# Kernel optimization log

Measured on AMD Instinct MI355X. Metric: run time of the kernel, lower is better.

Reference implementation:

```python
import jax, jax.numpy as jnp
import numpy as np


def setup_inputs() -> dict:
    key = jax.random.key(0)
    k1, k2 = jax.random.split(key)
    B, C, H, W, D = 2, 1, 128, 128, 128
    image = jax.random.normal(k1, (B, C, H, W, D), dtype=jnp.float32)
    # dense displacement field in voxel units (typical registration magnitudes)
    ddf = jax.random.normal(k2, (B, 3, H, W, D), dtype=jnp.float32) * 3.0
    return {"image": image, "ddf": ddf}


def _warp(image, ddf):
    """Trilinear grid_sample warp, padding_mode='zeros', align_corners=True.

    Equivalent to MONAI Warp(mode=1, padding_mode='zeros'): the reference grid
    plus DDF gives absolute voxel coordinates; torch's normalization to [-1,1]
    with align_corners=True followed by grid_sample maps exactly back to these
    voxel coordinates, so we sample directly in voxel space.
    """
    B, C, H, W, D = image.shape
    dt = image.dtype
    mesh = jnp.stack(
        jnp.meshgrid(
            jnp.arange(H, dtype=dt),
            jnp.arange(W, dtype=dt),
            jnp.arange(D, dtype=dt),
            indexing="ij",
        ),
        axis=-1,
    )  # (H, W, D, 3)
    coords = mesh[None] + jnp.moveaxis(ddf, 1, -1)  # (B, H, W, D, 3) voxel coords

    c0f = jnp.floor(coords)
    frac = coords - c0f                      # (B, H, W, D, 3)
    c0 = c0f.astype(jnp.int32)
    sizes = jnp.array([H, W, D], dtype=jnp.int32)
    strides = jnp.array([W * D, D, 1], dtype=jnp.int32)

    N = H * W * D
    img_flat = image.reshape(B, C, N)
    out = jnp.zeros((B, C, N), dtype=dt)
    # 8 trilinear taps; zeros padding => out-of-range taps contribute 0
    for dx in (0, 1):
        for dy in (0, 1):
            for dz in (0, 1):
                off = jnp.array([dx, dy, dz], dtype=jnp.int32)
                idx = c0 + off                                   # (B,H,W,D,3)
                wsel = jnp.where(off == 1, frac, 1.0 - frac)
                w = wsel[..., 0] * wsel[..., 1] * wsel[..., 2]   # (B,H,W,D)
                valid = jnp.all((idx >= 0) & (idx < sizes), axis=-1)
                idxc = jnp.clip(idx, 0, sizes - 1)
                lin = jnp.sum(idxc * strides, axis=-1).reshape(B, N)
                vals = jax.vmap(lambda im, li: im[:, li])(img_flat, lin)  # (B,C,N)
                out = out + vals * (w * valid.astype(dt)).reshape(B, 1, N)
    return out.reshape(B, C, H, W, D)


def reference(image, ddf):
    return _warp(image, ddf)
```

## Files before the change

kernel.cpp:

```cpp
#include <hip/hip_runtime.h>
#include <hip/hip_fp16.h>


constexpr int H = 128, W = 128, D = 128;
constexpr int N = H * W * D;
constexpr int B = 2;
constexpr int HA = 8;
constexpr int RS = 32;
constexpr int RCELL = 18;
constexpr int RHALF = RCELL * 2;
constexpr int RN = RS * RS * RHALF;

typedef float fvec4 __attribute__((ext_vector_type(4)));
typedef unsigned u2v __attribute__((ext_vector_type(2), aligned(4)));
typedef unsigned u2v8 __attribute__((ext_vector_type(2), aligned(8)));

__global__ __launch_bounds__(1024, 8) void warp_tile_kernel(
    const float* __restrict__ image,
    const float* __restrict__ ddf,
    float* __restrict__ out)
{
    __shared__ __half tile[RN];

    int bid = blockIdx.x;
    int T   = (bid & 7) * 128 + (bid >> 3);
    int b  = T >> 9;
    int t3 = T & 511;
    int tx0 = ((t3 >> 6) & 7) << 4;
    int ty0 = ((t3 >> 3) & 7) << 4;
    int tz0 = (t3 & 7) << 4;
    int ox = tx0 - HA, oy = ty0 - HA, oz = tz0 - HA;

    const float* img = image + ((size_t)b << 21);
    int t = threadIdx.x;

    int zq = (t & 3) << 2;
    int ly = (t >> 2) & 15;
    int lx = t >> 6;
    int vx = tx0 + lx, vy = ty0 + ly, vz = tz0 + zq;
    int lin0 = (vx << 14) + (vy << 7) + vz;

    fvec4 sa[4], sb[4];
    int rows[4], zos[4];
#pragma unroll
    for (int c = 0; c < 4; ++c) {
        int s   = c * 1024 + t;
        int row = s >> 2;
        int zo  = (s & 3) << 3;
        rows[c] = row; zos[c] = zo;
        int gx = ox + (row >> 5);
        int gy = oy + (row & 31);
        int gz = oz + zo;
        bool ok = ((unsigned)gx < 128u) & ((unsigned)gy < 128u) & ((unsigned)gz < 121u);
        const float* p = img + (gx << 14) + (gy << 7) + gz;
        fvec4 z4 = {0.f, 0.f, 0.f, 0.f};
        sa[c] = ok ? *(const fvec4*)p       : z4;
        sb[c] = ok ? *(const fvec4*)(p + 4) : z4;
    }

    const float* ddfb = ddf + (size_t)b * 3 * N;
    fvec4 dx4 = *(const fvec4*)(ddfb + lin0);
    fvec4 dy4 = *(const fvec4*)(ddfb + lin0 + N);
    fvec4 dz4 = *(const fvec4*)(ddfb + lin0 + 2 * N);

    unsigned short* tp = (unsigned short*)tile;
#pragma unroll
    for (int c = 0; c < 4; ++c) {
        __half2 h0 = __floats2half2_rn(sa[c].x, sa[c].y);
        __half2 h1 = __floats2half2_rn(sa[c].z, sa[c].w);
        __half2 h2 = __floats2half2_rn(sb[c].x, sb[c].y);
        __half2 h3 = __floats2half2_rn(sb[c].z, sb[c].w);
        u2v8 w0, w1;
        w0.x = *(unsigned int*)&h0;
        w0.y = *(unsigned int*)&h1;
        w1.x = *(unsigned int*)&h2;
        w1.y = *(unsigned int*)&h3;
        unsigned short* dst = tp + rows[c] * RHALF + zos[c];
        *(u2v8*)dst       = w0;
        *(u2v8*)(dst + 4) = w1;
    }
    __syncthreads();

    __builtin_amdgcn_s_setprio(1);

    float* outb = out + ((size_t)b << 21);
    const unsigned int* cells = (const unsigned int*)tile;
    float dxp[4] = {dx4.x, dx4.y, dx4.z, dx4.w};
    float dyp[4] = {dy4.x, dy4.y, dy4.z, dy4.w};
    float dzp[4] = {dz4.x, dz4.y, dz4.z, dz4.w};
    float res[4];

#pragma unroll
    for (int i = 0; i < 4; ++i) {
        float x = (float)vx + dxp[i];
        float y = (float)vy + dyp[i];
        float z = (float)(vz + i) + dzp[i];

        float xf = floorf(x), yf = floorf(y), zf = floorf(z);
        float fx = x - xf, fy = y - yf, fz = z - zf;
        int x0 = (int)xf, y0 = (int)yf, z0 = (int)zf;
        int rx = x0 - ox, ry = y0 - oy, rz = z0 - oz;

        float acc;
        if ((unsigned)rx <= 30u && (unsigned)ry <= 30u && (unsigned)rz <= 30u) {
            int row = (rx << 5) + ry;
            int c   = row * RCELL + (rz >> 1);
            int sh  = (rz & 1) << 4;
            u2v q00 = *(const u2v*)(cells + c);
            u2v q01 = *(const u2v*)(cells + c + RCELL);
            u2v q10 = *(const u2v*)(cells + c + 32 * RCELL);
            u2v q11 = *(const u2v*)(cells + c + 33 * RCELL);

            float az0 = 1.f - fz;
            float zz[4];
            unsigned los[4] = {q00.x, q01.x, q10.x, q11.x};
            unsigned his[4] = {q00.y, q01.y, q10.y, q11.y};
#pragma unroll
            for (int p2 = 0; p2 < 4; ++p2) {
                unsigned pr = __builtin_amdgcn_alignbit(his[p2], los[p2],
                                                        (unsigned)sh);
                __half2 hp = *(__half2*)&pr;
                float2 f2 = __half22float2(hp);
                zz[p2] = az0 * f2.x + fz * f2.y;
            }
            float ay0 = 1.f - fy;
            acc = (1.f - fx) * (ay0 * zz[0] + fy * zz[1]) +
                  fx         * (ay0 * zz[2] + fy * zz[3]);
        } else {
            int x1 = x0 + 1, y1 = y0 + 1, z1 = z0 + 1;
            bool vx0 = (unsigned)x0 < (unsigned)H;
            bool vx1 = (unsigned)x1 < (unsigned)H;
            bool vy0 = (unsigned)y0 < (unsigned)W;
            bool vy1 = (unsigned)y1 < (unsigned)W;
            bool vz0 = (unsigned)z0 < (unsigned)D;
            bool vz1 = (unsigned)z1 < (unsigned)D;
            float ax0 = vx0 ? (1.0f - fx) : 0.0f;
            float ax1 = vx1 ? fx          : 0.0f;
            float ay0 = vy0 ? (1.0f - fy) : 0.0f;
            float ay1 = vy1 ? fy          : 0.0f;
            float az0 = vz0 ? (1.0f - fz) : 0.0f;
            float az1 = vz1 ? fz          : 0.0f;
            int cx0 = vx0 ? x0 : 0;
            int cx1 = vx1 ? x1 : 0;
            int cy0 = vy0 ? y0 : 0;
            int cy1 = vy1 ? y1 : 0;
            int cz0 = vz0 ? z0 : 0;
            int cz1 = vz1 ? z1 : 0;
            int rx0 = cx0 << 14, rx1 = cx1 << 14;
            int ry0 = cy0 << 7,  ry1 = cy1 << 7;
            float v000 = img[rx0 + ry0 + cz0];
            float v001 = img[rx0 + ry0 + cz1];
            float v010 = img[rx0 + ry1 + cz0];
            float v011 = img[rx0 + ry1 + cz1];
            float v100 = img[rx1 + ry0 + cz0];
            float v101 = img[rx1 + ry0 + cz1];
            float v110 = img[rx1 + ry1 + cz0];
            float v111 = img[rx1 + ry1 + cz1];
            acc = ax0 * (ay0 * (az0 * v000 + az1 * v001) +
                         ay1 * (az0 * v010 + az1 * v011)) +
                  ax1 * (ay0 * (az0 * v100 + az1 * v101) +
                         ay1 * (az0 * v110 + az1 * v111));
        }
        res[i] = acc;
    }
    __builtin_amdgcn_s_setprio(0);
    fvec4 r4 = {res[0], res[1], res[2], res[3]};
    __builtin_nontemporal_store(r4, (fvec4*)(outb + lin0));
}

extern "C" void kernel_launch(void* const* d_in, const int* in_sizes, int n_in,
                              void* d_out, int out_size, void* d_ws, size_t ws_size,
                              hipStream_t stream) {
    const float* image = (const float*)d_in[0];
    const float* ddf   = (const float*)d_in[1];
    float* out = (float*)d_out;

    warp_tile_kernel<<<B * 512, 1024, 0, stream>>>(image, ddf, out);
}
```

Measured before the change: 102.5 us.

## Process two x-adjacent tiles per block with ring-buffered halo reuse

Each block now handles two consecutive 16-wide x tiles, with half the grid size. The shared-memory halo is indexed modulo 32 in x, so the second tile reuses 16 of the 32 loaded x-planes and loads only 16 new ones. The loads for the second tile's new planes are issued before the first tile's compute so their latency overlaps it. This cuts redundant halo loads from global memory and overlaps loading with compute, but it halves the number of blocks and adds extra barriers and register pressure.

```diff
diff --git a/kernel.cpp b/kernel.cpp
--- a/kernel.cpp
+++ b/kernel.cpp
@@ -5,11 +5,9 @@
 constexpr int H = 128, W = 128, D = 128;
 constexpr int N = H * W * D;
 constexpr int B = 2;
-constexpr int HA = 8;
-constexpr int RS = 32;
 constexpr int RCELL = 18;
 constexpr int RHALF = RCELL * 2;
-constexpr int RN = RS * RS * RHALF;
+constexpr int RN = 1024 * RHALF;
 
 typedef float fvec4 __attribute__((ext_vector_type(4)));
 typedef unsigned u2v __attribute__((ext_vector_type(2), aligned(4)));
@@ -23,149 +21,210 @@
     __shared__ __half tile[RN];
 
     int bid = blockIdx.x;
-    int T   = (bid & 7) * 128 + (bid >> 3);
-    int b  = T >> 9;
-    int t3 = T & 511;
-    int tx0 = ((t3 >> 6) & 7) << 4;
+    int T   = (bid & 7) * 64 + (bid >> 3);
+    int b   = T >> 8;
+    int t3  = T & 255;
+    int xcol = t3 >> 6;
     int ty0 = ((t3 >> 3) & 7) << 4;
     int tz0 = (t3 & 7) << 4;
-    int ox = tx0 - HA, oy = ty0 - HA, oz = tz0 - HA;
-
-    const float* img = image + ((size_t)b << 21);
+    int tx1 = xcol << 5;
+    int ox1 = tx1 - 8;
+    int oy  = ty0 - 8, oz = tz0 - 8;
+
+    const float* img  = image + ((size_t)b << 21);
+    float*       outb = out   + ((size_t)b << 21);
+    const float* ddfb = ddf + (size_t)b * 3 * N;
     int t = threadIdx.x;
 
     int zq = (t & 3) << 2;
     int ly = (t >> 2) & 15;
     int lx = t >> 6;
-    int vx = tx0 + lx, vy = ty0 + ly, vz = tz0 + zq;
-    int lin0 = (vx << 14) + (vy << 7) + vz;
-
-    fvec4 sa[4], sb[4];
-    int rows[4], zos[4];
-#pragma unroll
-    for (int c = 0; c < 4; ++c) {
-        int s   = c * 1024 + t;
-        int row = s >> 2;
-        int zo  = (s & 3) << 3;
-        rows[c] = row; zos[c] = zo;
-        int gx = ox + (row >> 5);
-        int gy = oy + (row & 31);
-        int gz = oz + zo;
-        bool ok = ((unsigned)gx < 128u) & ((unsigned)gy < 128u) & ((unsigned)gz < 121u);
-        const float* p = img + (gx << 14) + (gy << 7) + gz;
-        fvec4 z4 = {0.f, 0.f, 0.f, 0.f};
-        sa[c] = ok ? *(const fvec4*)p       : z4;
-        sb[c] = ok ? *(const fvec4*)(p + 4) : z4;
+    int vy = ty0 + ly, vz = tz0 + zq;
+    int vx1 = tx1 + lx;
+    int lin1 = (vx1 << 14) + (vy << 7) + vz;
+
+    const unsigned int* cells = (const unsigned int*)tile;
+    unsigned short* tp = (unsigned short*)tile;
+
+    auto compute_tile = [&](int vx, int ox, const fvec4& dX, const fvec4& dY,
+                            const fvec4& dZ, int lin) {
+        float dxp[4] = {dX.x, dX.y, dX.z, dX.w};
+        float dyp[4] = {dY.x, dY.y, dY.z, dY.w};
+        float dzp[4] = {dZ.x, dZ.y, dZ.z, dZ.w};
+        float res[4];
+        __builtin_amdgcn_s_setprio(1);
+#pragma unroll
+        for (int i = 0; i < 4; ++i) {
+            float x = (float)vx + dxp[i];
+            float y = (float)vy + dyp[i];
+            float z = (float)(vz + i) + dzp[i];
+
+            float xf = floorf(x), yf = floorf(y), zf = floorf(z);
+            float fx = x - xf, fy = y - yf, fz = z - zf;
+            int x0 = (int)xf, y0 = (int)yf, z0 = (int)zf;
+            int rx = x0 - ox, ry = y0 - oy, rz = z0 - oz;
+
+            float acc;
+            if ((unsigned)rx <= 30u && (unsigned)ry <= 30u && (unsigned)rz <= 30u) {
+                int r0 = ((x0 & 31) << 5) + ry;
+                int r1 = (((x0 + 1) & 31) << 5) + ry;
+                int czi = rz >> 1;
+                int sh  = (rz & 1) << 4;
+                int c00 = r0 * RCELL + czi;
+                int c10 = r1 * RCELL + czi;
+                u2v q00 = *(const u2v*)(cells + c00);
+                u2v q01 = *(const u2v*)(cells + c00 + RCELL);
+                u2v q10 = *(const u2v*)(cells + c10);
+                u2v q11 = *(const u2v*)(cells + c10 + RCELL);
+
+                float az0 = 1.f - fz;
+                float zz[4];
+                unsigned los[4] = {q00.x, q01.x, q10.x, q11.x};
+                unsigned his[4] = {q00.y, q01.y, q10.y, q11.y};
+#pragma unroll
+                for (int p2 = 0; p2 < 4; ++p2) {
+                    unsigned pr = __builtin_amdgcn_alignbit(his[p2], los[p2],
+                                                            (unsigned)sh);
+                    __half2 hp = *(__half2*)&pr;
+                    float2 f2 = __half22float2(hp);
+                    zz[p2] = az0 * f2.x + fz * f2.y;
+                }
+                float ay0 = 1.f - fy;
+                acc = (1.f - fx) * (ay0 * zz[0] + fy * zz[1]) +
+                      fx         * (ay0 * zz[2] + fy * zz[3]);
+            } else {
+                int x1 = x0 + 1, y1 = y0 + 1, z1 = z0 + 1;
+                bool vx0 = (unsigned)x0 < (unsigned)H;
+                bool vx1b = (unsigned)x1 < (unsigned)H;
+                bool vy0 = (unsigned)y0 < (unsigned)W;
+                bool vy1 = (unsigned)y1 < (unsigned)W;
+                bool vz0 = (unsigned)z0 < (unsigned)D;
+                bool vz1 = (unsigned)z1 < (unsigned)D;
+                float ax0 = vx0 ? (1.0f - fx) : 0.0f;
+                float ax1 = vx1b ? fx         : 0.0f;
+                float ay0 = vy0 ? (1.0f - fy) : 0.0f;
+                float ay1 = vy1 ? fy          : 0.0f;
+                float az0 = vz0 ? (1.0f - fz) : 0.0f;
+                float az1 = vz1 ? fz          : 0.0f;
+                int cx0 = vx0 ? x0 : 0;
+                int cx1 = vx1b ? x1 : 0;
+                int cy0 = vy0 ? y0 : 0;
+                int cy1 = vy1 ? y1 : 0;
+                int cz0 = vz0 ? z0 : 0;
+                int cz1 = vz1 ? z1 : 0;
+                int rx0 = cx0 << 14, rx1i = cx1 << 14;
+                int ry0 = cy0 << 7,  ry1 = cy1 << 7;
+                float v000 = img[rx0 + ry0 + cz0];
+                float v001 = img[rx0 + ry0 + cz1];
+                float v010 = img[rx0 + ry1 + cz0];
+                float v011 = img[rx0 + ry1 + cz1];
+                float v100 = img[rx1i + ry0 + cz0];
+                float v101 = img[rx1i + ry0 + cz1];
+                float v110 = img[rx1i + ry1 + cz0];
+                float v111 = img[rx1i + ry1 + cz1];
+                acc = ax0 * (ay0 * (az0 * v000 + az1 * v001) +
+                             ay1 * (az0 * v010 + az1 * v011)) +
+                      ax1 * (ay0 * (az0 * v100 + az1 * v101) +
+                             ay1 * (az0 * v110 + az1 * v111));
+            }
+            res[i] = acc;
+        }
+        __builtin_amdgcn_s_setprio(0);
+        fvec4 r4 = {res[0], res[1], res[2], res[3]};
+        __builtin_nontemporal_store(r4, (fvec4*)(outb + lin));
+    };
+
+    {
+        fvec4 sa[4], sb[4];
+        int srow[4], zos[4];
+#pragma unroll
+        for (int c = 0; c < 4; ++c) {
+            int s   = c * 1024 + t;
+            int row = s >> 2;
+            int p   = row >> 5;
+            int yy  = row & 31;
+            int zo  = (s & 3) << 3;
+            int gx = ox1 + p;
+            int gy = oy + yy;
+            int gz = oz + zo;
+            srow[c] = ((gx & 31) << 5) + yy;
+            zos[c]  = zo;
+            bool ok = ((unsigned)gx < 128u) & ((unsigned)gy < 128u) & ((unsigned)gz < 121u);
+            const float* pp = img + (gx << 14) + (gy << 7) + gz;
+            fvec4 z4 = {0.f, 0.f, 0.f, 0.f};
+            sa[c] = ok ? *(const fvec4*)pp       : z4;
+            sb[c] = ok ? *(const fvec4*)(pp + 4) : z4;
+        }
+        fvec4 dxa = *(const fvec4*)(ddfb + lin1);
+        fvec4 dya = *(const fvec4*)(ddfb + lin1 + N);
+        fvec4 dza = *(const fvec4*)(ddfb + lin1 + 2 * N);
+
+#pragma unroll
+        for (int c = 0; c < 4; ++c) {
+            __half2 h0 = __floats2half2_rn(sa[c].x, sa[c].y);
+            __half2 h1 = __floats2half2_rn(sa[c].z, sa[c].w);
+            __half2 h2 = __floats2half2_rn(sb[c].x, sb[c].y);
+            __half2 h3 = __floats2half2_rn(sb[c].z, sb[c].w);
+            u2v8 w0, w1;
+            w0.x = *(unsigned int*)&h0;
+            w0.y = *(unsigned int*)&h1;
+            w1.x = *(unsigned int*)&h2;
+            w1.y = *(unsigned int*)&h3;
+            unsigned short* dst = tp + srow[c] * RHALF + zos[c];
+            *(u2v8*)dst       = w0;
+            *(u2v8*)(dst + 4) = w1;
+        }
+        __syncthreads();
+
+        fvec4 s2a[2], s2b[2];
+        int srow2[2], zos2[2];
+#pragma unroll
+        for (int c = 0; c < 2; ++c) {
+            int s   = c * 1024 + t;
+            int row = s >> 2;
+            int p   = row >> 5;
+            int yy  = row & 31;
+            int zo  = (s & 3) << 3;
+            int gx = tx1 + 24 + p;
+            int gy = oy + yy;
+            int gz = oz + zo;
+            srow2[c] = ((gx & 31) << 5) + yy;
+            zos2[c]  = zo;
+            bool ok = ((unsigned)gx < 128u) & ((unsigned)gy < 128u) & ((unsigned)gz < 121u);
+            const float* pp = img + (gx << 14) + (gy << 7) + gz;
+            fvec4 z4 = {0.f, 0.f, 0.f, 0.f};
+            s2a[c] = ok ? *(const fvec4*)pp       : z4;
+            s2b[c] = ok ? *(const fvec4*)(pp + 4) : z4;
+        }
+
+        compute_tile(vx1, ox1, dxa, dya, dza, lin1);
+
+        __syncthreads();
+
+        int lin2 = lin1 + (16 << 14);
+        fvec4 dxb = *(const fvec4*)(ddfb + lin2);
+        fvec4 dyb = *(const fvec4*)(ddfb + lin2 + N);
+        fvec4 dzb = *(const fvec4*)(ddfb + lin2 + 2 * N);
+
+#pragma unroll
+        for (int c = 0; c < 2; ++c) {
+            __half2 h0 = __floats2half2_rn(s2a[c].x, s2a[c].y);
+            __half2 h1 = __floats2half2_rn(s2a[c].z, s2a[c].w);
+            __half2 h2 = __floats2half2_rn(s2b[c].x, s2b[c].y);
+            __half2 h3 = __floats2half2_rn(s2b[c].z, s2b[c].w);
+            u2v8 w0, w1;
+            w0.x = *(unsigned int*)&h0;
+            w0.y = *(unsigned int*)&h1;
+            w1.x = *(unsigned int*)&h2;
+            w1.y = *(unsigned int*)&h3;
+            unsigned short* dst = tp + srow2[c] * RHALF + zos2[c];
+            *(u2v8*)dst       = w0;
+            *(u2v8*)(dst + 4) = w1;
+        }
+        __syncthreads();
+
+        compute_tile(vx1 + 16, ox1 + 16, dxb, dyb, dzb, lin2);
     }
-
-    const float* ddfb = ddf + (size_t)b * 3 * N;
-    fvec4 dx4 = *(const fvec4*)(ddfb + lin0);
-    fvec4 dy4 = *(const fvec4*)(ddfb + lin0 + N);
-    fvec4 dz4 = *(const fvec4*)(ddfb + lin0 + 2 * N);
-
-    unsigned short* tp = (unsigned short*)tile;
-#pragma unroll
-    for (int c = 0; c < 4; ++c) {
-        __half2 h0 = __floats2half2_rn(sa[c].x, sa[c].y);
-        __half2 h1 = __floats2half2_rn(sa[c].z, sa[c].w);
-        __half2 h2 = __floats2half2_rn(sb[c].x, sb[c].y);
-        __half2 h3 = __floats2half2_rn(sb[c].z, sb[c].w);
-        u2v8 w0, w1;
-        w0.x = *(unsigned int*)&h0;
-        w0.y = *(unsigned int*)&h1;
-        w1.x = *(unsigned int*)&h2;
-        w1.y = *(unsigned int*)&h3;
-        unsigned short* dst = tp + rows[c] * RHALF + zos[c];
-        *(u2v8*)dst       = w0;
-        *(u2v8*)(dst + 4) = w1;
-    }
-    __syncthreads();
-
-    __builtin_amdgcn_s_setprio(1);
-
-    float* outb = out + ((size_t)b << 21);
-    const unsigned int* cells = (const unsigned int*)tile;
-    float dxp[4] = {dx4.x, dx4.y, dx4.z, dx4.w};
-    float dyp[4] = {dy4.x, dy4.y, dy4.z, dy4.w};
-    float dzp[4] = {dz4.x, dz4.y, dz4.z, dz4.w};
-    float res[4];
-
-#pragma unroll
-    for (int i = 0; i < 4; ++i) {
-        float x = (float)vx + dxp[i];
-        float y = (float)vy + dyp[i];
-        float z = (float)(vz + i) + dzp[i];
-
-        float xf = floorf(x), yf = floorf(y), zf = floorf(z);
-        float fx = x - xf, fy = y - yf, fz = z - zf;
-        int x0 = (int)xf, y0 = (int)yf, z0 = (int)zf;
-        int rx = x0 - ox, ry = y0 - oy, rz = z0 - oz;
-
-        float acc;
-        if ((unsigned)rx <= 30u && (unsigned)ry <= 30u && (unsigned)rz <= 30u) {
-            int row = (rx << 5) + ry;
-            int c   = row * RCELL + (rz >> 1);
-            int sh  = (rz & 1) << 4;
-            u2v q00 = *(const u2v*)(cells + c);
-            u2v q01 = *(const u2v*)(cells + c + RCELL);
-            u2v q10 = *(const u2v*)(cells + c + 32 * RCELL);
-            u2v q11 = *(const u2v*)(cells + c + 33 * RCELL);
-
-            float az0 = 1.f - fz;
-            float zz[4];
-            unsigned los[4] = {q00.x, q01.x, q10.x, q11.x};
-            unsigned his[4] = {q00.y, q01.y, q10.y, q11.y};
-#pragma unroll
-            for (int p2 = 0; p2 < 4; ++p2) {
-                unsigned pr = __builtin_amdgcn_alignbit(his[p2], los[p2],
-                                                        (unsigned)sh);
-                __half2 hp = *(__half2*)&pr;
-                float2 f2 = __half22float2(hp);
-                zz[p2] = az0 * f2.x + fz * f2.y;
-            }
-            float ay0 = 1.f - fy;
-            acc = (1.f - fx) * (ay0 * zz[0] + fy * zz[1]) +
-                  fx         * (ay0 * zz[2] + fy * zz[3]);
-        } else {
-            int x1 = x0 + 1, y1 = y0 + 1, z1 = z0 + 1;
-            bool vx0 = (unsigned)x0 < (unsigned)H;
-            bool vx1 = (unsigned)x1 < (unsigned)H;
-            bool vy0 = (unsigned)y0 < (unsigned)W;
-            bool vy1 = (unsigned)y1 < (unsigned)W;
-            bool vz0 = (unsigned)z0 < (unsigned)D;
-            bool vz1 = (unsigned)z1 < (unsigned)D;
-            float ax0 = vx0 ? (1.0f - fx) : 0.0f;
-            float ax1 = vx1 ? fx          : 0.0f;
-            float ay0 = vy0 ? (1.0f - fy) : 0.0f;
-            float ay1 = vy1 ? fy          : 0.0f;
-            float az0 = vz0 ? (1.0f - fz) : 0.0f;
-            float az1 = vz1 ? fz          : 0.0f;
-            int cx0 = vx0 ? x0 : 0;
-            int cx1 = vx1 ? x1 : 0;
-            int cy0 = vy0 ? y0 : 0;
-            int cy1 = vy1 ? y1 : 0;
-            int cz0 = vz0 ? z0 : 0;
-            int cz1 = vz1 ? z1 : 0;
-            int rx0 = cx0 << 14, rx1 = cx1 << 14;
-            int ry0 = cy0 << 7,  ry1 = cy1 << 7;
-            float v000 = img[rx0 + ry0 + cz0];
-            float v001 = img[rx0 + ry0 + cz1];
-            float v010 = img[rx0 + ry1 + cz0];
-            float v011 = img[rx0 + ry1 + cz1];
-            float v100 = img[rx1 + ry0 + cz0];
-            float v101 = img[rx1 + ry0 + cz1];
-            float v110 = img[rx1 + ry1 + cz0];
-            float v111 = img[rx1 + ry1 + cz1];
-            acc = ax0 * (ay0 * (az0 * v000 + az1 * v001) +
-                         ay1 * (az0 * v010 + az1 * v011)) +
-                  ax1 * (ay0 * (az0 * v100 + az1 * v101) +
-                         ay1 * (az0 * v110 + az1 * v111));
-        }
-        res[i] = acc;
-    }
-    __builtin_amdgcn_s_setprio(0);
-    fvec4 r4 = {res[0], res[1], res[2], res[3]};
-    __builtin_nontemporal_store(r4, (fvec4*)(outb + lin0));
 }
 
 extern "C" void kernel_launch(void* const* d_in, const int* in_sizes, int n_in,
@@ -175,5 +234,5 @@
     const float* ddf   = (const float*)d_in[1];
     float* out = (float*)d_out;
 
-    warp_tile_kernel<<<B * 512, 1024, 0, stream>>>(image, ddf, out);
+    warp_tile_kernel<<<B * 256, 1024, 0, stream>>>(image, ddf, out);
 }
```

Result: slower. 111.3 us (+8.6%).
